# Kernel tuning notes

Measured on AMD Instinct MI355X. Metric: run time of the kernel, lower is better.

## Reference

```python
import jax, jax.numpy as jnp
import numpy as np

N = 100000      # nodes
E = 1600000     # edges (avg degree 16)
G = 1000        # graphs in batch
F_IN = 128      # num_features
C = 10          # num_classes
EPS = 1e-5


def setup_inputs() -> dict:
    key = jax.random.key(0)
    ks = jax.random.split(key, 12)
    w = lambda k, shape: jax.random.normal(k, shape, jnp.float32) * 0.05
    return {
        'x': jax.random.normal(ks[0], (N, F_IN), jnp.float32),
        'edge_index': jax.random.randint(ks[1], (2, E), 0, N, jnp.int32),
        'edge_weights': jax.random.randint(ks[2], (E,), 0, 2, jnp.int32),
        'batch': jnp.sort(jax.random.randint(ks[3], (N,), 0, G, jnp.int32)),
        'num_graphs': G,
        # initial MLP: Linear(128,32)+BN+ReLU, Linear(32,32)+BN+ReLU
        'W1': w(ks[4], (F_IN, 32)), 'b1': jnp.zeros(32), 'g1': jnp.ones(32), 'bt1': jnp.zeros(32),
        'W2': w(ks[5], (32, 32)), 'b2': jnp.zeros(32), 'g2': jnp.ones(32), 'bt2': jnp.zeros(32),
        'Wl0': w(ks[6], (32, C)), 'bl0': jnp.zeros(C),   # initial_linear
        'Wg1': w(ks[7], (32, 64)), 'bg1': jnp.zeros(64),  # GCNConv 1
        'Wl1': w(ks[8], (64, C)), 'bl1': jnp.zeros(C),
        'Wg2': w(ks[9], (64, 64)), 'bg2': jnp.zeros(64),  # GCNConv 2
        'Wl2': w(ks[10], (64, C)), 'bl2': jnp.zeros(C),
    }


def _bn(h, gamma, beta):
    # BatchNorm1d in training mode: biased batch statistics over nodes
    mu = h.mean(0)
    var = ((h - mu) ** 2).mean(0)
    return gamma * (h - mu) * jax.lax.rsqrt(var + EPS) + beta


def _gcn(h_in, row, col, w, W, b):
    # PyG GCNConv with self-loops: D^{-1/2}(A+I)D^{-1/2} X W + b,
    # edges with mask weight 0 contribute nothing (incl. to degree).
    n = h_in.shape[0]
    h = h_in @ W
    deg = jax.ops.segment_sum(w, col, num_segments=n) + 1.0  # +1 self-loop
    dinv = jax.lax.rsqrt(deg)
    norm = w * dinv[row] * dinv[col]                  # [E]
    agg = jax.ops.segment_sum(h[row] * norm[:, None], col, num_segments=n)
    agg = agg + h * (dinv * dinv)[:, None]            # self-loop term
    return agg + b


def _pool_max(h, batch, num_graphs):
    # torch_scatter scatter_max readout; empty segments -> 0
    p = jax.ops.segment_max(h, batch, num_segments=num_graphs)
    return jnp.where(jnp.isfinite(p), p, 0.0)


def reference(x, edge_index, edge_weights, batch, num_graphs,
              W1, b1, g1, bt1, W2, b2, g2, bt2, Wl0, bl0,
              Wg1, bg1, Wl1, bl1, Wg2, bg2, Wl2, bl2):
    row, col = edge_index[0], edge_index[1]
    w = (edge_weights == 1).astype(x.dtype)  # boolean edge mask as 0/1 weight
    # initial MLP (dropout treated as identity for deterministic reference)
    h = jax.nn.relu(_bn(x @ W1 + b1, g1, bt1))
    h = jax.nn.relu(_bn(h @ W2 + b2, g2, bt2))
    out = _pool_max(h @ Wl0 + bl0, batch, num_graphs)
    # layer 1
    h = _gcn(h, row, col, w, Wg1, bg1)
    out = out + _pool_max(h, batch, num_graphs) @ Wl1 + bl1
    # layer 2
    h = _gcn(h, row, col, w, Wg2, bg2)
    out = out + _pool_max(h, batch, num_graphs) @ Wl2 + bl2
    return out
```

## Files before the change

### kernel.cpp

```cpp
#include <hip/hip_runtime.h>

#define NN 100000
#define EE 1600000
#define GG 1000
#define BN_EPS 1e-5f
#define NTB 782
#define SLOT 64

__device__ __forceinline__ unsigned encf(float f){
  unsigned u = __float_as_uint(f);
  return (u & 0x80000000u) ? ~u : (u | 0x80000000u);
}
__device__ __forceinline__ float dec0(unsigned e){
  unsigned u = (e & 0x80000000u) ? (e & 0x7fffffffu) : ~e;
  float f = __uint_as_float(u);
  return isfinite(f) ? f : 0.0f;
}
__device__ __forceinline__ unsigned short f2bf(float f){
  unsigned u = __float_as_uint(f);
  u += 0x7FFFu + ((u >> 16) & 1u);
  return (unsigned short)(u >> 16);
}
__device__ __forceinline__ float bf2f(unsigned short s){
  return __uint_as_float(((unsigned)s) << 16);
}

#define STEP4(AX, WV) \
  acc[0][0]=fmaf(a0.AX,WV.x,acc[0][0]); acc[0][1]=fmaf(a0.AX,WV.y,acc[0][1]); \
  acc[0][2]=fmaf(a0.AX,WV.z,acc[0][2]); acc[0][3]=fmaf(a0.AX,WV.w,acc[0][3]); \
  acc[1][0]=fmaf(a1.AX,WV.x,acc[1][0]); acc[1][1]=fmaf(a1.AX,WV.y,acc[1][1]); \
  acc[1][2]=fmaf(a1.AX,WV.z,acc[1][2]); acc[1][3]=fmaf(a1.AX,WV.w,acc[1][3]); \
  acc[2][0]=fmaf(a2.AX,WV.x,acc[2][0]); acc[2][1]=fmaf(a2.AX,WV.y,acc[2][1]); \
  acc[2][2]=fmaf(a2.AX,WV.z,acc[2][2]); acc[2][3]=fmaf(a2.AX,WV.w,acc[2][3]); \
  acc[3][0]=fmaf(a3.AX,WV.x,acc[3][0]); acc[3][1]=fmaf(a3.AX,WV.y,acc[3][1]); \
  acc[3][2]=fmaf(a3.AX,WV.z,acc[3][2]); acc[3][3]=fmaf(a3.AX,WV.w,acc[3][3]);

__global__ void k_scatter(const int* __restrict__ ei, const int* __restrict__ ew,
                          int* __restrict__ fill, int* __restrict__ csr,
                          const float* __restrict__ x, unsigned short* __restrict__ Xb){
  const int t = blockIdx.x*256 + threadIdx.x;
  if (t < EE && ew[t] == 1){
    int c = ei[EE + t];
    int pos = atomicAdd(&fill[c], 1);
    if (pos < SLOT) csr[(size_t)c*SLOT + pos] = ei[t];
  }
  const size_t base = (size_t)t * 2;
  #pragma unroll
  for (int i = 0; i < 2; i++){
    const size_t idx = base + i;
    if (idx < (size_t)NN*32){
      float4 v = ((const float4*)x)[idx];
      ushort4 u; u.x=f2bf(v.x); u.y=f2bf(v.y); u.z=f2bf(v.z); u.w=f2bf(v.w);
      ((ushort4*)Xb)[idx] = u;
    }
  }
}

__global__ void k_dinv(const int* __restrict__ fill, float* __restrict__ dinv){
  int i = blockIdx.x*256 + threadIdx.x;
  if (i < NN) dinv[i] = rsqrtf((float)fill[i] + 1.0f);
}

__global__ __launch_bounds__(256) void k_gemm1(const unsigned short* __restrict__ Xb,
    const float* __restrict__ W1, const float* __restrict__ b1,
    unsigned short* __restrict__ Y1b, float* __restrict__ stats){
  __shared__ unsigned short xs[128*136];
  __shared__ unsigned short Ws[128*32];
  __shared__ float red[64];
  const int tid = threadIdx.x;
  if (tid < 64) red[tid] = 0.f;
  #pragma unroll
  for (int j = 0; j < 4; j++){
    int idx = tid + j*256;
    int kk = idx >> 3, cc = idx & 7;
    float4 w = ((const float4*)W1)[(size_t)kk*8 + cc];
    ushort4 u; u.x=f2bf(w.x); u.y=f2bf(w.y); u.z=f2bf(w.z); u.w=f2bf(w.w);
    *(ushort4*)&Ws[kk*32 + cc*4] = u;
  }
  const long rowbase = (long)blockIdx.x*128;
  for (int j = tid; j < 4096; j += 256){
    int rr = j >> 5, kk = j & 31;
    long gr = rowbase + rr;
    ushort4 u = (gr < NN) ? ((const ushort4*)Xb)[gr*32 + kk] : ushort4{0,0,0,0};
    *(ushort4*)&xs[rr*136 + kk*4] = u;
  }
  __syncthreads();
  const int rg = tid >> 3, cg = tid & 7;
  const float4 bv = ((const float4*)b1)[cg];
  float acc[4][4];
  #pragma unroll
  for (int i = 0; i < 4; i++){ acc[i][0]=bv.x; acc[i][1]=bv.y; acc[i][2]=bv.z; acc[i][3]=bv.w; }
  #pragma unroll 4
  for (int k = 0; k < 128; k += 4){
    const ushort4 u0 = *(const ushort4*)&xs[(rg     )*136 + k];
    const ushort4 u1 = *(const ushort4*)&xs[(rg + 32)*136 + k];
    const ushort4 u2 = *(const ushort4*)&xs[(rg + 64)*136 + k];
    const ushort4 u3 = *(const ushort4*)&xs[(rg + 96)*136 + k];
    float4 a0, a1, a2, a3;
    a0.x=bf2f(u0.x); a0.y=bf2f(u0.y); a0.z=bf2f(u0.z); a0.w=bf2f(u0.w);
    a1.x=bf2f(u1.x); a1.y=bf2f(u1.y); a1.z=bf2f(u1.z); a1.w=bf2f(u1.w);
    a2.x=bf2f(u2.x); a2.y=bf2f(u2.y); a2.z=bf2f(u2.z); a2.w=bf2f(u2.w);
    a3.x=bf2f(u3.x); a3.y=bf2f(u3.y); a3.z=bf2f(u3.z); a3.w=bf2f(u3.w);
    const ushort4 wu0 = *(const ushort4*)&Ws[(k+0)*32 + cg*4];
    const ushort4 wu1 = *(const ushort4*)&Ws[(k+1)*32 + cg*4];
    const ushort4 wu2 = *(const ushort4*)&Ws[(k+2)*32 + cg*4];
    const ushort4 wu3 = *(const ushort4*)&Ws[(k+3)*32 + cg*4];
    float4 w0, w1, w2, w3;
    w0.x=bf2f(wu0.x); w0.y=bf2f(wu0.y); w0.z=bf2f(wu0.z); w0.w=bf2f(wu0.w);
    w1.x=bf2f(wu1.x); w1.y=bf2f(wu1.y); w1.z=bf2f(wu1.z); w1.w=bf2f(wu1.w);
    w2.x=bf2f(wu2.x); w2.y=bf2f(wu2.y); w2.z=bf2f(wu2.z); w2.w=bf2f(wu2.w);
    w3.x=bf2f(wu3.x); w3.y=bf2f(wu3.y); w3.z=bf2f(wu3.z); w3.w=bf2f(wu3.w);
    STEP4(x, w0) STEP4(y, w1) STEP4(z, w2) STEP4(w, w3)
  }
  float s[4] = {0,0,0,0}, q[4] = {0,0,0,0};
  #pragma unroll
  for (int i = 0; i < 4; i++){
    const long r = rowbase + rg + 32*i;
    if (r < NN){
      ushort4 o; o.x=f2bf(acc[i][0]); o.y=f2bf(acc[i][1]); o.z=f2bf(acc[i][2]); o.w=f2bf(acc[i][3]);
      ((ushort4*)Y1b)[r*8 + cg] = o;
      #pragma unroll
      for (int j = 0; j < 4; j++){ s[j] += acc[i][j]; q[j] += acc[i][j]*acc[i][j]; }
    }
  }
  __syncthreads();
  #pragma unroll
  for (int j = 0; j < 4; j++){
    atomicAdd(&red[cg*4+j], s[j]);
    atomicAdd(&red[32+cg*4+j], q[j]);
  }
  __syncthreads();
  if (tid < 64) atomicAdd(&stats[tid], red[tid]);
}

__global__ __launch_bounds__(256) void k_mlp2(const unsigned short* __restrict__ Y1b,
    const float* __restrict__ W2, const float* __restrict__ b2,
    const float* __restrict__ g1, const float* __restrict__ bt1,
    float* __restrict__ stats, unsigned short* __restrict__ Y2b){
  __shared__ float ht[128*36];
  __shared__ float Ws[32*32];
  __shared__ float red[64];
  __shared__ float scs[32], shs[32];
  const int tid = threadIdx.x;
  ((float4*)Ws)[tid] = ((const float4*)W2)[tid];
  if (tid < 64) red[tid] = 0.f;
  if (tid < 32){
    float mean = stats[tid] * (1.0f/NN);
    float var  = stats[32 + tid] * (1.0f/NN) - mean*mean;
    float sH = g1[tid] * rsqrtf(fmaxf(var, 0.0f) + BN_EPS);
    scs[tid] = sH; shs[tid] = bt1[tid] - mean*sH;
  }
  __syncthreads();
  const long rowbase = (long)blockIdx.x*128;
  for (int j = tid; j < 1024; j += 256){
    int rr = j >> 3, kk = j & 7;
    long gr = rowbase + rr;
    ushort4 u = (gr < NN) ? ((const ushort4*)Y1b)[gr*8 + kk] : ushort4{0,0,0,0};
    float4 v;
    v.x = fmaxf(fmaf(bf2f(u.x), scs[kk*4+0], shs[kk*4+0]), 0.f);
    v.y = fmaxf(fmaf(bf2f(u.y), scs[kk*4+1], shs[kk*4+1]), 0.f);
    v.z = fmaxf(fmaf(bf2f(u.z), scs[kk*4+2], shs[kk*4+2]), 0.f);
    v.w = fmaxf(fmaf(bf2f(u.w), scs[kk*4+3], shs[kk*4+3]), 0.f);
    *(float4*)&ht[rr*36 + kk*4] = v;
  }
  __syncthreads();
  const int rg = tid >> 3, cg = tid & 7;
  const float4 bv = ((const float4*)b2)[cg];
  float acc[4][4];
  #pragma unroll
  for (int i = 0; i < 4; i++){ acc[i][0]=bv.x; acc[i][1]=bv.y; acc[i][2]=bv.z; acc[i][3]=bv.w; }
  #pragma unroll
  for (int k = 0; k < 32; k += 4){
    const float4 a0 = *(const float4*)&ht[(rg     )*36 + k];
    const float4 a1 = *(const float4*)&ht[(rg + 32)*36 + k];
    const float4 a2 = *(const float4*)&ht[(rg + 64)*36 + k];
    const float4 a3 = *(const float4*)&ht[(rg + 96)*36 + k];
    const float4 w0 = *(const float4*)&Ws[(k+0)*32 + cg*4];
    const float4 w1 = *(const float4*)&Ws[(k+1)*32 + cg*4];
    const float4 w2 = *(const float4*)&Ws[(k+2)*32 + cg*4];
    const float4 w3 = *(const float4*)&Ws[(k+3)*32 + cg*4];
    STEP4(x, w0) STEP4(y, w1) STEP4(z, w2) STEP4(w, w3)
  }
  float s[4] = {0,0,0,0}, q[4] = {0,0,0,0};
  #pragma unroll
  for (int i = 0; i < 4; i++){
    const long r = rowbase + rg + 32*i;
    if (r < NN){
      ushort4 o; o.x=f2bf(acc[i][0]); o.y=f2bf(acc[i][1]); o.z=f2bf(acc[i][2]); o.w=f2bf(acc[i][3]);
      ((ushort4*)Y2b)[r*8 + cg] = o;
      #pragma unroll
      for (int j = 0; j < 4; j++){ s[j] += acc[i][j]; q[j] += acc[i][j]*acc[i][j]; }
    }
  }
  __syncthreads();
  #pragma unroll
  for (int j = 0; j < 4; j++){
    atomicAdd(&red[cg*4+j], s[j]);
    atomicAdd(&red[32+cg*4+j], q[j]);
  }
  __syncthreads();
  if (tid < 64) atomicAdd(&stats[128 + tid], red[tid]);
}

__global__ __launch_bounds__(256) void k_layer0(const unsigned short* __restrict__ Y2b,
    const float* __restrict__ stats, const float* __restrict__ g2,
    const float* __restrict__ bt2, const float* __restrict__ Wg1,
    const float* __restrict__ Wl0, const float* __restrict__ bl0,
    const float* __restrict__ dinv, const int* __restrict__ batch,
    unsigned short* __restrict__ Hs1, unsigned* __restrict__ Pool0){
  __shared__ float hs[32*36];
  __shared__ float Wg[32*64];
  __shared__ float Wl[320];
  __shared__ float bl[10];
  __shared__ float scs[32], shs[32];
  const int tid = threadIdx.x;
  ((float4*)Wg)[tid]       = ((const float4*)Wg1)[tid];
  ((float4*)Wg)[tid + 256] = ((const float4*)Wg1)[tid + 256];
  for (int j = tid; j < 320; j += 256) Wl[j] = Wl0[j];
  if (tid < 10)  bl[tid] = bl0[tid];
  if (tid < 32){
    float mean = stats[128 + tid] * (1.0f/NN);
    float var  = stats[160 + tid] * (1.0f/NN) - mean*mean;
    float s = g2[tid] * rsqrtf(fmaxf(var, 0.0f) + BN_EPS);
    scs[tid] = s; shs[tid] = bt2[tid] - mean*s;
  }
  __syncthreads();
  {
    const int rr = tid >> 3, kk = tid & 7;
    const float4 sc = *(const float4*)&scs[kk*4];
    const float4 sh = *(const float4*)&shs[kk*4];
    ushort4 u = ((const ushort4*)Y2b)[(size_t)blockIdx.x*256 + tid];
    float4 v;
    v.x = fmaxf(fmaf(bf2f(u.x), sc.x, sh.x), 0.f);
    v.y = fmaxf(fmaf(bf2f(u.y), sc.y, sh.y), 0.f);
    v.z = fmaxf(fmaf(bf2f(u.z), sc.z, sh.z), 0.f);
    v.w = fmaxf(fmaf(bf2f(u.w), sc.w, sh.w), 0.f);
    *(float4*)&hs[rr*36 + kk*4] = v;
  }
  __syncthreads();
  const int w = tid >> 6, f = tid & 63;
  for (int i = 0; i < 8; i++){
    const int r = w*8 + i;
    const int row = blockIdx.x*32 + r;
    const float* hr = &hs[r*36];
    float acc = 0.f;
    #pragma unroll
    for (int k = 0; k < 32; k++) acc += hr[k]*Wg[k*64 + f];
    Hs1[(size_t)row*64 + f] = f2bf(acc * dinv[row]);
    if (f < 10){
      float p = bl[f];
      #pragma unroll
      for (int k = 0; k < 32; k++) p += hr[k]*Wl[k*10 + f];
      atomicMax(&Pool0[batch[row]*10 + f], encf(p));
    }
  }
}

__device__ __forceinline__ float gather_sum(const unsigned short* __restrict__ Hs,
    const int* __restrict__ csr, int s, int e, int f){
  float acc = 0.f;
  int j = s;
  for (; j + 7 < e; j += 8){
    const int r0 = csr[j],   r1 = csr[j+1], r2 = csr[j+2], r3 = csr[j+3];
    const int r4 = csr[j+4], r5 = csr[j+5], r6 = csr[j+6], r7 = csr[j+7];
    float t0 = bf2f(Hs[(size_t)r0*64 + f]);
    float t1 = bf2f(Hs[(size_t)r1*64 + f]);
    float t2 = bf2f(Hs[(size_t)r2*64 + f]);
    float t3 = bf2f(Hs[(size_t)r3*64 + f]);
    float t4 = bf2f(Hs[(size_t)r4*64 + f]);
    float t5 = bf2f(Hs[(size_t)r5*64 + f]);
    float t6 = bf2f(Hs[(size_t)r6*64 + f]);
    float t7 = bf2f(Hs[(size_t)r7*64 + f]);
    acc += ((t0 + t1) + (t2 + t3)) + ((t4 + t5) + (t6 + t7));
  }
  for (; j + 3 < e; j += 4){
    const int r0 = csr[j], r1 = csr[j+1], r2 = csr[j+2], r3 = csr[j+3];
    float t0 = bf2f(Hs[(size_t)r0*64 + f]);
    float t1 = bf2f(Hs[(size_t)r1*64 + f]);
    float t2 = bf2f(Hs[(size_t)r2*64 + f]);
    float t3 = bf2f(Hs[(size_t)r3*64 + f]);
    acc += (t0 + t1) + (t2 + t3);
  }
  for (; j < e; j++) acc += bf2f(Hs[(size_t)csr[j]*64 + f]);
  return acc;
}

__device__ __forceinline__ void pool_epilogue(float h, int w, int f, int c,
    const int* __restrict__ batch, unsigned* __restrict__ Pool,
    float (*sm)[64], int* sb){
  sm[w][f] = h;
  if (f == 0) sb[w] = batch[c];
  __syncthreads();
  if (w == 0){
    const int b0 = sb[0], b1 = sb[1], b2 = sb[2], b3 = sb[3];
    if (b0 == b3){
      float m = fmaxf(fmaxf(sm[0][f], sm[1][f]), fmaxf(sm[2][f], sm[3][f]));
      atomicMax(&Pool[b0*64 + f], encf(m));
    } else {
      atomicMax(&Pool[b0*64 + f], encf(sm[0][f]));
      atomicMax(&Pool[b1*64 + f], encf(sm[1][f]));
      atomicMax(&Pool[b2*64 + f], encf(sm[2][f]));
      atomicMax(&Pool[b3*64 + f], encf(sm[3][f]));
    }
  }
}

__global__ __launch_bounds__(256) void k_agg1(const unsigned short* __restrict__ Hs,
    const float* __restrict__ dinv, const int* __restrict__ fill,
    const int* __restrict__ csr, const float* __restrict__ bias,
    const int* __restrict__ batch, unsigned short* __restrict__ H2b,
    unsigned* __restrict__ Pool){
  __shared__ float sm[4][64];
  __shared__ int sb[4];
  const int w = threadIdx.x >> 6, f = threadIdx.x & 63;
  const int c = blockIdx.x*4 + w;
  const int n = min(fill[c], SLOT);
  const int s = c*SLOT;
  float acc = gather_sum(Hs, csr, s, s + n, f);
  const float dc = dinv[c];
  const float h = fmaf(acc + bf2f(Hs[(size_t)c*64 + f]), dc, bias[f]);
  H2b[(size_t)c*64 + f] = f2bf(h);
  pool_epilogue(h, w, f, c, batch, Pool, sm, sb);
}

__global__ __launch_bounds__(256) void k_agg2(const unsigned short* __restrict__ Hs,
    const float* __restrict__ dinv, const int* __restrict__ fill,
    const int* __restrict__ csr, const float* __restrict__ bias,
    const int* __restrict__ batch, unsigned* __restrict__ Pool){
  __shared__ float sm[4][64];
  __shared__ int sb[4];
  const int w = threadIdx.x >> 6, f = threadIdx.x & 63;
  const int c = blockIdx.x*4 + w;
  const int n = min(fill[c], SLOT);
  const int s = c*SLOT;
  float acc = gather_sum(Hs, csr, s, s + n, f);
  const float dc = dinv[c];
  const float h = fmaf(acc + bf2f(Hs[(size_t)c*64 + f]), dc, bias[f]);
  pool_epilogue(h, w, f, c, batch, Pool, sm, sb);
}

__global__ __launch_bounds__(256) void k_layer1(const unsigned short* __restrict__ H2b,
    const float* __restrict__ Wg2, const float* __restrict__ dinv,
    unsigned short* __restrict__ Hs2){
  __shared__ float as[32*68];
  __shared__ float Wg[64*64];
  const int tid = threadIdx.x;
  #pragma unroll
  for (int j = 0; j < 4; j++) ((float4*)Wg)[tid + j*256] = ((const float4*)Wg2)[tid + j*256];
  {
    const int rr = tid >> 3, kk = tid & 7;
    ushort4 v0 = ((const ushort4*)H2b)[(size_t)blockIdx.x*512 + tid*2];
    ushort4 v1 = ((const ushort4*)H2b)[(size_t)blockIdx.x*512 + tid*2 + 1];
    float* dst = &as[rr*68 + kk*8];
    dst[0]=bf2f(v0.x); dst[1]=bf2f(v0.y); dst[2]=bf2f(v0.z); dst[3]=bf2f(v0.w);
    dst[4]=bf2f(v1.x); dst[5]=bf2f(v1.y); dst[6]=bf2f(v1.z); dst[7]=bf2f(v1.w);
  }
  __syncthreads();
  const int w = tid >> 6, f = tid & 63;
  for (int i = 0; i < 8; i++){
    const int r = w*8 + i;
    const int row = blockIdx.x*32 + r;
    const float* ar = &as[r*68];
    float acc = 0.f;
    #pragma unroll
    for (int k = 0; k < 64; k++) acc += ar[k]*Wg[k*64 + f];
    Hs2[(size_t)row*64 + f] = f2bf(acc * dinv[row]);
  }
}

__global__ __launch_bounds__(256) void k_final(const unsigned* __restrict__ P0,
    const unsigned* __restrict__ P1, const unsigned* __restrict__ P2,
    const float* __restrict__ Wl1, const float* __restrict__ bl1,
    const float* __restrict__ Wl2, const float* __restrict__ bl2,
    float* __restrict__ out){
  const int t = blockIdx.x*256 + threadIdx.x;
  const int g = t >> 4, c = t & 15;
  if (g >= GG || c >= 10) return;
  float acc = dec0(P0[g*10 + c]) + bl1[c] + bl2[c];
  for (int f = 0; f < 64; f++){
    acc += dec0(P1[g*64 + f]) * Wl1[f*10 + c];
    acc += dec0(P2[g*64 + f]) * Wl2[f*10 + c];
  }
  out[g*10 + c] = acc;
}

extern "C" void kernel_launch(void* const* d_in, const int* in_sizes, int n_in,
                              void* d_out, int out_size, void* d_ws, size_t ws_size,
                              hipStream_t stream){
  const float* x   = (const float*)d_in[0];
  const int*   ei  = (const int*)d_in[1];
  const int*   ew  = (const int*)d_in[2];
  const int*   bat = (const int*)d_in[3];
  const float* W1  = (const float*)d_in[5],  *b1  = (const float*)d_in[6];
  const float* g1  = (const float*)d_in[7],  *bt1 = (const float*)d_in[8];
  const float* W2  = (const float*)d_in[9],  *b2  = (const float*)d_in[10];
  const float* g2  = (const float*)d_in[11], *bt2 = (const float*)d_in[12];
  const float* Wl0 = (const float*)d_in[13], *bl0 = (const float*)d_in[14];
  const float* Wg1 = (const float*)d_in[15], *bg1 = (const float*)d_in[16];
  const float* Wl1 = (const float*)d_in[17], *bl1 = (const float*)d_in[18];
  const float* Wg2 = (const float*)d_in[19], *bg2 = (const float*)d_in[20];
  const float* Wl2 = (const float*)d_in[21], *bl2 = (const float*)d_in[22];

  float* ws = (float*)d_ws;
  const size_t oFill  = 0;
  const size_t oStats = NN;
  const size_t oP0    = oStats + 256;
  const size_t oP1    = oP0 + (size_t)GG*10;
  const size_t oP2    = oP1 + (size_t)GG*64;
  const size_t oZEnd  = oP2 + (size_t)GG*64;
  const size_t oDinv  = oZEnd;
  const size_t oCsr   = oDinv + NN;
  const size_t oR1    = oCsr + (size_t)NN*SLOT;
  const size_t oR2    = oR1 + (size_t)NN*16;
  const size_t oR3    = oR2 + (size_t)NN*16;
  const size_t oR4    = oR3 + (size_t)NN*32;

  int*   fill  = (int*)(ws + oFill);
  float* stats = ws + oStats;
  unsigned* P0 = (unsigned*)(ws + oP0);
  unsigned* P1 = (unsigned*)(ws + oP1);
  unsigned* P2 = (unsigned*)(ws + oP2);
  float* dinv  = ws + oDinv;
  int*   csr   = (int*)(ws + oCsr);
  unsigned short* Y1b = (unsigned short*)(ws + oR1);
  unsigned short* Y2b = (unsigned short*)(ws + oR2);
  unsigned short* Xb  = (unsigned short*)(ws + oR3);
  unsigned short* Hs1 = (unsigned short*)(ws + oR3);
  unsigned short* Hs2 = (unsigned short*)(ws + oR3);
  unsigned short* H2b = (unsigned short*)(ws + oR4);

  (void)hipMemsetAsync(d_ws, 0, oZEnd*sizeof(float), stream);

  k_scatter<<<EE/256, 256, 0, stream>>>(ei, ew, fill, csr, x, Xb);
  k_dinv   <<<(NN + 255)/256, 256, 0, stream>>>(fill, dinv);
  k_gemm1<<<NTB, 256, 0, stream>>>(Xb, W1, b1, Y1b, stats);
  k_mlp2 <<<NTB, 256, 0, stream>>>(Y1b, W2, b2, g1, bt1, stats, Y2b);
  k_layer0<<<3125, 256, 0, stream>>>(Y2b, stats, g2, bt2, Wg1, Wl0, bl0, dinv, bat, Hs1, P0);
  k_agg1 <<<NN/4, 256, 0, stream>>>(Hs1, dinv, fill, csr, bg1, bat, H2b, P1);
  k_layer1<<<3125, 256, 0, stream>>>(H2b, Wg2, dinv, Hs2);
  k_agg2 <<<NN/4, 256, 0, stream>>>(Hs2, dinv, fill, csr, bg2, bat, P2);
  k_final<<<(GG*16 + 255)/256, 256, 0, stream>>>(P0, P1, P2, Wl1, bl1, Wl2, bl2, (float*)d_out);
}
```

Measured before the change: 297.5 us.

## Store gathered GCN features as scaled 8-bit floats and inline degree counts in CSR

Gathered per-node features Hs1/Hs2 are now stored in a custom 8-bit float format (4-bit exponent, 3-bit mantissa, pre-scaled by 16) instead of bf16. This halves the bytes moved by the random-access neighbour gathers. The separate fill/degree array is dropped: the count now sits in slot 0 of each node's CSR row, which needs a full memset of the CSR buffer and leaves one fewer neighbour slot per node. The price is a large precision loss in aggregation, extra decode ALU per gathered element, and a much bigger memset.

```diff
diff --git a/kernel.cpp b/kernel.cpp
--- a/kernel.cpp
+++ b/kernel.cpp
@@ -23,6 +23,32 @@
 }
 __device__ __forceinline__ float bf2f(unsigned short s){
   return __uint_as_float(((unsigned)s) << 16);
+}
+__device__ __forceinline__ unsigned char f2q(float f){
+  unsigned u = __float_as_uint(f);
+  unsigned s = (u >> 24) & 0x80u;
+  int e = (int)((u >> 23) & 0xFF);
+  unsigned m = u & 0x7FFFFFu;
+  int e8 = e - 120;
+  if (e8 >= 1){
+    unsigned mm = m >> 20;
+    unsigned rest = m & 0xFFFFFu;
+    mm += (rest > 0x80000u) || (rest == 0x80000u && (mm & 1u));
+    if (mm == 8u){ mm = 0u; e8++; }
+    return (unsigned char)(s | ((unsigned)e8 << 3) | mm);
+  } else {
+    float av = fabsf(f) * 512.0f;
+    int q = (int)rintf(av); if (q > 7) q = 7;
+    return (unsigned char)(s | (unsigned)q);
+  }
+}
+__device__ __forceinline__ float q2f(unsigned char b){
+  unsigned s = ((unsigned)b & 0x80u) << 24;
+  unsigned e = ((unsigned)b >> 3) & 0xFu;
+  unsigned m = (unsigned)b & 7u;
+  float vn = __uint_as_float(s | ((e + 120u) << 23) | (m << 20));
+  float vs = __uint_as_float(s | 0x3F800000u) * (float)m * 0.001953125f;
+  return e ? vn : vs;
 }
 
 #define STEP4(AX, WV) \
@@ -36,13 +62,13 @@
   acc[3][2]=fmaf(a3.AX,WV.z,acc[3][2]); acc[3][3]=fmaf(a3.AX,WV.w,acc[3][3]);
 
 __global__ void k_scatter(const int* __restrict__ ei, const int* __restrict__ ew,
-                          int* __restrict__ fill, int* __restrict__ csr,
+                          int* __restrict__ csr,
                           const float* __restrict__ x, unsigned short* __restrict__ Xb){
   const int t = blockIdx.x*256 + threadIdx.x;
   if (t < EE && ew[t] == 1){
     int c = ei[EE + t];
-    int pos = atomicAdd(&fill[c], 1);
-    if (pos < SLOT) csr[(size_t)c*SLOT + pos] = ei[t];
+    int pos = atomicAdd(&csr[(size_t)c*SLOT], 1);
+    if (pos < SLOT-1) csr[(size_t)c*SLOT + 1 + pos] = ei[t];
   }
   const size_t base = (size_t)t * 2;
   #pragma unroll
@@ -56,9 +82,9 @@
   }
 }
 
-__global__ void k_dinv(const int* __restrict__ fill, float* __restrict__ dinv){
+__global__ void k_dinv(const int* __restrict__ csr, float* __restrict__ dinv){
   int i = blockIdx.x*256 + threadIdx.x;
-  if (i < NN) dinv[i] = rsqrtf((float)fill[i] + 1.0f);
+  if (i < NN) dinv[i] = rsqrtf((float)csr[(size_t)i*SLOT] + 1.0f);
 }
 
 __global__ __launch_bounds__(256) void k_gemm1(const unsigned short* __restrict__ Xb,
@@ -207,7 +233,7 @@
     const float* __restrict__ bt2, const float* __restrict__ Wg1,
     const float* __restrict__ Wl0, const float* __restrict__ bl0,
     const float* __restrict__ dinv, const int* __restrict__ batch,
-    unsigned short* __restrict__ Hs1, unsigned* __restrict__ Pool0){
+    unsigned char* __restrict__ Hs1, unsigned* __restrict__ Pool0){
   __shared__ float hs[32*36];
   __shared__ float Wg[32*64];
   __shared__ float Wl[320];
@@ -246,7 +272,7 @@
     float acc = 0.f;
     #pragma unroll
     for (int k = 0; k < 32; k++) acc += hr[k]*Wg[k*64 + f];
-    Hs1[(size_t)row*64 + f] = f2bf(acc * dinv[row]);
+    Hs1[(size_t)row*64 + f] = f2q(acc * dinv[row] * 16.0f);
     if (f < 10){
       float p = bl[f];
       #pragma unroll
@@ -256,32 +282,32 @@
   }
 }
 
-__device__ __forceinline__ float gather_sum(const unsigned short* __restrict__ Hs,
+__device__ __forceinline__ float gather_sum(const unsigned char* __restrict__ Hs,
     const int* __restrict__ csr, int s, int e, int f){
   float acc = 0.f;
   int j = s;
   for (; j + 7 < e; j += 8){
     const int r0 = csr[j],   r1 = csr[j+1], r2 = csr[j+2], r3 = csr[j+3];
     const int r4 = csr[j+4], r5 = csr[j+5], r6 = csr[j+6], r7 = csr[j+7];
-    float t0 = bf2f(Hs[(size_t)r0*64 + f]);
-    float t1 = bf2f(Hs[(size_t)r1*64 + f]);
-    float t2 = bf2f(Hs[(size_t)r2*64 + f]);
-    float t3 = bf2f(Hs[(size_t)r3*64 + f]);
-    float t4 = bf2f(Hs[(size_t)r4*64 + f]);
-    float t5 = bf2f(Hs[(size_t)r5*64 + f]);
-    float t6 = bf2f(Hs[(size_t)r6*64 + f]);
-    float t7 = bf2f(Hs[(size_t)r7*64 + f]);
+    float t0 = q2f(Hs[(size_t)r0*64 + f]);
+    float t1 = q2f(Hs[(size_t)r1*64 + f]);
+    float t2 = q2f(Hs[(size_t)r2*64 + f]);
+    float t3 = q2f(Hs[(size_t)r3*64 + f]);
+    float t4 = q2f(Hs[(size_t)r4*64 + f]);
+    float t5 = q2f(Hs[(size_t)r5*64 + f]);
+    float t6 = q2f(Hs[(size_t)r6*64 + f]);
+    float t7 = q2f(Hs[(size_t)r7*64 + f]);
     acc += ((t0 + t1) + (t2 + t3)) + ((t4 + t5) + (t6 + t7));
   }
   for (; j + 3 < e; j += 4){
     const int r0 = csr[j], r1 = csr[j+1], r2 = csr[j+2], r3 = csr[j+3];
-    float t0 = bf2f(Hs[(size_t)r0*64 + f]);
-    float t1 = bf2f(Hs[(size_t)r1*64 + f]);
-    float t2 = bf2f(Hs[(size_t)r2*64 + f]);
-    float t3 = bf2f(Hs[(size_t)r3*64 + f]);
+    float t0 = q2f(Hs[(size_t)r0*64 + f]);
+    float t1 = q2f(Hs[(size_t)r1*64 + f]);
+    float t2 = q2f(Hs[(size_t)r2*64 + f]);
+    float t3 = q2f(Hs[(size_t)r3*64 + f]);
     acc += (t0 + t1) + (t2 + t3);
   }
-  for (; j < e; j++) acc += bf2f(Hs[(size_t)csr[j]*64 + f]);
+  for (; j < e; j++) acc += q2f(Hs[(size_t)csr[j]*64 + f]);
   return acc;
 }
 
@@ -305,43 +331,42 @@
   }
 }
 
-__global__ __launch_bounds__(256) void k_agg1(const unsigned short* __restrict__ Hs,
-    const float* __restrict__ dinv, const int* __restrict__ fill,
-    const int* __restrict__ csr, const float* __restrict__ bias,
-    const int* __restrict__ batch, unsigned short* __restrict__ H2b,
+__global__ __launch_bounds__(256) void k_agg1(const unsigned char* __restrict__ Hs,
+    const float* __restrict__ dinv, const int* __restrict__ csr,
+    const float* __restrict__ bias, const int* __restrict__ batch,
+    unsigned short* __restrict__ H2b, unsigned* __restrict__ Pool){
+  __shared__ float sm[4][64];
+  __shared__ int sb[4];
+  const int w = threadIdx.x >> 6, f = threadIdx.x & 63;
+  const int c = blockIdx.x*4 + w;
+  const int s = c*SLOT;
+  const int n = min(csr[s], SLOT-1);
+  float acc = gather_sum(Hs, csr, s + 1, s + 1 + n, f);
+  const float dc = dinv[c];
+  const float h = fmaf(acc + q2f(Hs[(size_t)c*64 + f]), dc*0.0625f, bias[f]);
+  H2b[(size_t)c*64 + f] = f2bf(h);
+  pool_epilogue(h, w, f, c, batch, Pool, sm, sb);
+}
+
+__global__ __launch_bounds__(256) void k_agg2(const unsigned char* __restrict__ Hs,
+    const float* __restrict__ dinv, const int* __restrict__ csr,
+    const float* __restrict__ bias, const int* __restrict__ batch,
     unsigned* __restrict__ Pool){
   __shared__ float sm[4][64];
   __shared__ int sb[4];
   const int w = threadIdx.x >> 6, f = threadIdx.x & 63;
   const int c = blockIdx.x*4 + w;
-  const int n = min(fill[c], SLOT);
   const int s = c*SLOT;
-  float acc = gather_sum(Hs, csr, s, s + n, f);
+  const int n = min(csr[s], SLOT-1);
+  float acc = gather_sum(Hs, csr, s + 1, s + 1 + n, f);
   const float dc = dinv[c];
-  const float h = fmaf(acc + bf2f(Hs[(size_t)c*64 + f]), dc, bias[f]);
-  H2b[(size_t)c*64 + f] = f2bf(h);
-  pool_epilogue(h, w, f, c, batch, Pool, sm, sb);
-}
-
-__global__ __launch_bounds__(256) void k_agg2(const unsigned short* __restrict__ Hs,
-    const float* __restrict__ dinv, const int* __restrict__ fill,
-    const int* __restrict__ csr, const float* __restrict__ bias,
-    const int* __restrict__ batch, unsigned* __restrict__ Pool){
-  __shared__ float sm[4][64];
-  __shared__ int sb[4];
-  const int w = threadIdx.x >> 6, f = threadIdx.x & 63;
-  const int c = blockIdx.x*4 + w;
-  const int n = min(fill[c], SLOT);
-  const int s = c*SLOT;
-  float acc = gather_sum(Hs, csr, s, s + n, f);
-  const float dc = dinv[c];
-  const float h = fmaf(acc + bf2f(Hs[(size_t)c*64 + f]), dc, bias[f]);
+  const float h = fmaf(acc + q2f(Hs[(size_t)c*64 + f]), dc*0.0625f, bias[f]);
   pool_epilogue(h, w, f, c, batch, Pool, sm, sb);
 }
 
 __global__ __launch_bounds__(256) void k_layer1(const unsigned short* __restrict__ H2b,
     const float* __restrict__ Wg2, const float* __restrict__ dinv,
-    unsigned short* __restrict__ Hs2){
+    unsigned char* __restrict__ Hs2){
   __shared__ float as[32*68];
   __shared__ float Wg[64*64];
   const int tid = threadIdx.x;
@@ -364,7 +389,7 @@
     float acc = 0.f;
     #pragma unroll
     for (int k = 0; k < 64; k++) acc += ar[k]*Wg[k*64 + f];
-    Hs2[(size_t)row*64 + f] = f2bf(acc * dinv[row]);
+    Hs2[(size_t)row*64 + f] = f2q(acc * dinv[row] * 16.0f);
   }
 }
 
@@ -402,8 +427,7 @@
   const float* Wl2 = (const float*)d_in[21], *bl2 = (const float*)d_in[22];
 
   float* ws = (float*)d_ws;
-  const size_t oFill  = 0;
-  const size_t oStats = NN;
+  const size_t oStats = 0;
   const size_t oP0    = oStats + 256;
   const size_t oP1    = oP0 + (size_t)GG*10;
   const size_t oP2    = oP1 + (size_t)GG*64;
@@ -415,7 +439,6 @@
   const size_t oR3    = oR2 + (size_t)NN*16;
   const size_t oR4    = oR3 + (size_t)NN*32;
 
-  int*   fill  = (int*)(ws + oFill);
   float* stats = ws + oStats;
   unsigned* P0 = (unsigned*)(ws + oP0);
   unsigned* P1 = (unsigned*)(ws + oP1);
@@ -425,19 +448,20 @@
   unsigned short* Y1b = (unsigned short*)(ws + oR1);
   unsigned short* Y2b = (unsigned short*)(ws + oR2);
   unsigned short* Xb  = (unsigned short*)(ws + oR3);
-  unsigned short* Hs1 = (unsigned short*)(ws + oR3);
-  unsigned short* Hs2 = (unsigned short*)(ws + oR3);
+  unsigned char*  Hs1 = (unsigned char*)(ws + oR3);
+  unsigned char*  Hs2 = (unsigned char*)(ws + oR3);
   unsigned short* H2b = (unsigned short*)(ws + oR4);
 
   (void)hipMemsetAsync(d_ws, 0, oZEnd*sizeof(float), stream);
-
-  k_scatter<<<EE/256, 256, 0, stream>>>(ei, ew, fill, csr, x, Xb);
-  k_dinv   <<<(NN + 255)/256, 256, 0, stream>>>(fill, dinv);
+  (void)hipMemsetAsync((void*)csr, 0, (size_t)NN*SLOT*sizeof(int), stream);
+
+  k_scatter<<<EE/256, 256, 0, stream>>>(ei, ew, csr, x, Xb);
+  k_dinv   <<<(NN + 255)/256, 256, 0, stream>>>(csr, dinv);
   k_gemm1<<<NTB, 256, 0, stream>>>(Xb, W1, b1, Y1b, stats);
   k_mlp2 <<<NTB, 256, 0, stream>>>(Y1b, W2, b2, g1, bt1, stats, Y2b);
   k_layer0<<<3125, 256, 0, stream>>>(Y2b, stats, g2, bt2, Wg1, Wl0, bl0, dinv, bat, Hs1, P0);
-  k_agg1 <<<NN/4, 256, 0, stream>>>(Hs1, dinv, fill, csr, bg1, bat, H2b, P1);
+  k_agg1 <<<NN/4, 256, 0, stream>>>(Hs1, dinv, csr, bg1, bat, H2b, P1);
   k_layer1<<<3125, 256, 0, stream>>>(H2b, Wg2, dinv, Hs2);
-  k_agg2 <<<NN/4, 256, 0, stream>>>(Hs2, dinv, fill, csr, bg2, bat, P2);
+  k_agg2 <<<NN/4, 256, 0, stream>>>(Hs2, dinv, csr, bg2, bat, P2);
   k_final<<<(GG*16 + 255)/256, 256, 0, stream>>>(P0, P1, P2, Wl1, bl1, Wl2, bl2, (float*)d_out);
 }
```

New measurement: 322.4 us. +8.4%, slower.
